# Optimization experiments

Hardware: AMD Instinct MI355X
Metric: run time of the kernel (lower is better)

The kernel has to match this reference:

```python
import jax, jax.numpy as jnp
import numpy as np

Q_LATTICE = 4      # nested lattice alphabet size
QMAX_ACT = 127.0   # 2**(8-1) - 1 for 8-bit LSQ


def _lattice_quantize(x_blocks, G, Ginv, q):
    # x_blocks: [N, 8] rows are block vectors. Lattice point = z @ G, z integer.
    z = jnp.round(x_blocks @ Ginv)
    half = q // 2
    z_mod = jnp.mod(z + half, q) - half  # nested (mod-q) lattice, centered
    return z_mod @ G


def setup_inputs() -> dict:
    key = jax.random.key(0)
    k1, k2 = jax.random.split(key)
    O, I, BS = 4096, 4096, 8
    rng = np.random.default_rng(0)
    G_np = np.eye(BS, dtype=np.float64) + 0.1 * rng.standard_normal((BS, BS))
    Ginv_np = np.linalg.inv(G_np)
    return {
        "x": jax.random.normal(k1, (256, I), dtype=jnp.float32),
        "weight": jax.random.normal(k2, (O, I), dtype=jnp.float32),
        "bias": jnp.zeros((O,), dtype=jnp.float32),
        "theta_beta": jnp.ones((O, 1), dtype=jnp.float32),
        "alpha": jnp.ones((1,), dtype=jnp.float32),
        "G": jnp.asarray(G_np, dtype=jnp.float32),
        "Ginv": jnp.asarray(Ginv_np, dtype=jnp.float32),
    }


def reference(x, weight, bias, theta_beta, alpha, G, Ginv):
    O, I = weight.shape
    bs = G.shape[0]
    nblk = I // bs
    sg = jax.lax.stop_gradient

    # --- hierarchical nested-lattice weight quantization (row tiling) ---
    W_blocks = weight.reshape(O, nblk, bs)
    # theta_beta [O, k] -> mean over k -> [O, 1, 1], broadcast to all blocks
    scale_w = jnp.mean(theta_beta, axis=-1, keepdims=True)[:, None, :]
    W_scaled = (W_blocks * scale_w).reshape(-1, bs)
    # straight-through lattice quantize
    W_q = W_scaled + sg(_lattice_quantize(W_scaled, G, Ginv, Q_LATTICE) - W_scaled)
    W_q = W_q.reshape(O, I)

    # --- linear ---
    y = x @ W_q.T + bias

    # --- LSQ activation quantization ---
    a = jax.nn.relu(alpha) + 1e-8          # [1]
    y_clipped = y + sg(jnp.clip(y, -a, a) - y)  # ste_clip (clamp detached)
    s = a / QMAX_ACT
    y_scaled = y_clipped / s
    y_round = y_scaled + sg(jnp.round(y_scaled) - y_scaled)  # ste_round
    return y_round * s
```

## Files before the change

kernel.cpp:

```cpp
#include <hip/hip_runtime.h>

typedef __attribute__((ext_vector_type(8))) __bf16 bf16x8;
typedef __attribute__((ext_vector_type(4))) float f32x4;

#define M_ 256
#define N_ 4096
#define K_ 4096
#define SPLITK 4
#define KC (K_ / SPLITK)
#define BM 256
#define BN 64
#define BK 32
#define KSTEPS (KC / BK)
#define NCH 36
#define LDSBUF 36864



__device__ __forceinline__ unsigned short f2bf(float f) {
  unsigned int u = __builtin_bit_cast(unsigned int, f);
  u += 0x7fffu + ((u >> 16) & 1u);
  return (unsigned short)(u >> 16);
}

__device__ __forceinline__ void async16(const void* g, void* l) {
  __builtin_amdgcn_global_load_lds(
      (const __attribute__((address_space(1))) unsigned int*)g,
      (__attribute__((address_space(3))) unsigned int*)l, 16, 0, 0);
}

__device__ __forceinline__ float lsq1(float y, float a, float s) {
  float yc = fminf(fmaxf(y, -a), a);
  return rintf(yc / s) * s;
}

#define ZLUT 0x3F800000BF80C000ull

__device__ __forceinline__ uint4 zdec(unsigned int w) {
  unsigned int d[4];
#pragma unroll
  for (int p = 0; p < 4; ++p) {
    const unsigned int lo = (unsigned int)((ZLUT >> (((w >> (4 * p)) & 3u) * 16)) & 0xFFFFull);
    const unsigned int hi = (unsigned int)((ZLUT >> (((w >> (4 * p + 2)) & 3u) * 16)) & 0xFFFFull);
    d[p] = lo | (hi << 16);
  }
  return make_uint4(d[0], d[1], d[2], d[3]);
}


#define NQB ((N_ * K_ / 8) / 256)
#define NXB ((M_ * K_ / 8) / 256)

__global__ __launch_bounds__(256) void k_prep(const float* __restrict__ W,
                                              const float* __restrict__ theta,
                                              const float* __restrict__ Ginv,
                                              const float* __restrict__ x,
                                              const float* __restrict__ G,
                                              unsigned short* __restrict__ z2,
                                              unsigned short* __restrict__ hi,
                                              unsigned short* __restrict__ lo,
                                              int kTheta) {
  __shared__ float Ms[64];
  const int tid = threadIdx.x;
  const bool isQ = blockIdx.x < NQB;
  if (tid < 64) Ms[tid] = isQ ? Ginv[tid] : G[tid];
  __syncthreads();

  if (isQ) {
#pragma clang fp contract(off)
    const int s = blockIdx.x * 256 + tid;
    const int lane6 = s & 63;
    const int tile = s >> 6;
    const int o  = ((tile >> 7) << 4) + (lane6 & 15);
    const int kb = ((tile & 127) << 2) + (lane6 >> 4);
    const float4* wp = (const float4*)(W + ((size_t)o << 12) + ((size_t)kb << 3));
    const float4 w0 = wp[0], w1 = wp[1];
    float sc = 0.f;
    for (int t = 0; t < kTheta; ++t) sc += theta[o * kTheta + t];
    sc /= (float)kTheta;
    const float wsv[8] = {w0.x * sc, w0.y * sc, w0.z * sc, w0.w * sc,
                          w1.x * sc, w1.y * sc, w1.z * sc, w1.w * sc};
    unsigned int word = 0u;
#pragma unroll
    for (int i = 0; i < 8; ++i) {
      float t = 0.f;
#pragma unroll
      for (int j = 0; j < 8; ++j)
        t = t + wsv[j] * Ms[j * 8 + i];
      const int zi = (int)rintf(t);
      word |= (unsigned int)((zi + 2) & 3) << (2 * i);
    }
    z2[s] = (unsigned short)word;
  } else {
    const int s = (blockIdx.x - NQB) * 256 + tid;
    const int lane6 = s & 63;
    const int tile = s >> 6;
    const int m  = ((tile >> 7) << 4) + (lane6 & 15);
    const int kb = ((tile & 127) << 2) + (lane6 >> 4);
    const float4* xp = (const float4*)(x + ((size_t)m << 12) + ((size_t)kb << 3));
    const float4 a0 = xp[0], a1 = xp[1];
    float xv[8] = {a0.x, a0.y, a0.z, a0.w, a1.x, a1.y, a1.z, a1.w};
    unsigned int ph[4] = {0u, 0u, 0u, 0u}, pl[4] = {0u, 0u, 0u, 0u};
#pragma unroll
    for (int i = 0; i < 8; ++i) {
      float t = 0.f;
#pragma unroll
      for (int j = 0; j < 8; ++j) t = fmaf(xv[j], Ms[i * 8 + j], t);
      const unsigned short hb = f2bf(t);
      const float hf = __builtin_bit_cast(float, (unsigned int)hb << 16);
      const unsigned short lb = f2bf(t - hf);
      ph[i >> 1] |= ((unsigned int)hb) << ((i & 1) * 16);
      pl[i >> 1] |= ((unsigned int)lb) << ((i & 1) * 16);
    }
    *(uint4*)(hi + ((size_t)s << 3)) = make_uint4(ph[0], ph[1], ph[2], ph[3]);
    *(uint4*)(lo + ((size_t)s << 3)) = make_uint4(pl[0], pl[1], pl[2], pl[3]);
  }
}


__global__ __launch_bounds__(512, 2) void k_gemm(const unsigned short* __restrict__ xgh,
                                                 const unsigned short* __restrict__ xgl,
                                                 const unsigned short* __restrict__ z2,
                                                 float* __restrict__ part) {
  __shared__ uint4 smem4[2 * LDSBUF / 16];
  char* smem = (char*)smem4;

  const int tid = threadIdx.x;
  const int lane = tid & 63, wave = tid >> 6;
  const int b = blockIdx.x;
  const int sk = b & 3;
  const int nt = b >> 2;
  const int k0t = sk * (KC / 32);
  const int lrow = lane & 15, lkg = lane >> 4;

  const unsigned short* asrc[4];
  int aldo[4];
#pragma unroll
  for (int ci = 0; ci < 4; ++ci) {
    const int c = wave * 4 + ci;
    const unsigned short* P = (c < 16) ? xgh : xgl;
    const int rt = c & 15;
    asrc[ci] = P + (((size_t)(rt * 128 + k0t)) << 9) + lane * 8;
    aldo[ci] = c * 1024;
  }
  const bool brole = (wave < 4);
  const unsigned short* zsrc = nullptr;
  int bofs = 0;
  if (brole) {
    zsrc = z2 + (((size_t)((nt * 4 + wave) * 128 + k0t)) << 6) + lane;
    bofs = (32 + wave) * 1024 + lane * 16;
  }

  f32x4 acc[2][4] = {};

  unsigned int zw = 0;
#pragma unroll
  for (int ci = 0; ci < 4; ++ci) async16(asrc[ci], smem + aldo[ci]);
  if (brole) {
    zw = zsrc[0];
    *(uint4*)(smem + bofs) = zdec(zw);
    zw = zsrc[64];
  }
  __syncthreads();

  for (int ks = 0; ks < KSTEPS; ++ks) {
    const int cur = (ks & 1) * LDSBUF;
    const int nxt = LDSBUF - cur;
    if (ks + 1 < KSTEPS) {
#pragma unroll
      for (int ci = 0; ci < 4; ++ci)
        async16(asrc[ci] + (size_t)(ks + 1) * 512, smem + nxt + aldo[ci]);
      if (brole) {
        *(uint4*)(smem + nxt + bofs) = zdec(zw);
        if (ks + 2 < KSTEPS) zw = zsrc[(size_t)(ks + 2) * 64];
      }
    }

    bf16x8 ah[2], al[2], bfr[4];
#pragma unroll
    for (int mf = 0; mf < 2; ++mf) {
      ah[mf] = *(const bf16x8*)(smem + cur + (wave * 2 + mf) * 1024 + lane * 16);
      al[mf] = *(const bf16x8*)(smem + cur + 16384 + (wave * 2 + mf) * 1024 + lane * 16);
    }
#pragma unroll
    for (int nf = 0; nf < 4; ++nf)
      bfr[nf] = *(const bf16x8*)(smem + cur + 32768 + nf * 1024 + lane * 16);

#pragma unroll
    for (int mf = 0; mf < 2; ++mf)
#pragma unroll
      for (int nf = 0; nf < 4; ++nf) {
        acc[mf][nf] = __builtin_amdgcn_mfma_f32_16x16x32_bf16(ah[mf], bfr[nf], acc[mf][nf], 0, 0, 0);
        acc[mf][nf] = __builtin_amdgcn_mfma_f32_16x16x32_bf16(al[mf], bfr[nf], acc[mf][nf], 0, 0, 0);
      }
    __syncthreads();
  }

  float* pb = part + (size_t)sk * (M_ * N_);
#pragma unroll
  for (int mf = 0; mf < 2; ++mf)
#pragma unroll
    for (int nf = 0; nf < 4; ++nf)
#pragma unroll
      for (int r = 0; r < 4; ++r) {
        const int m = wave * 32 + mf * 16 + lkg * 4 + r;
        const int n = nt * BN + nf * 16 + lrow;
        pb[(size_t)m * N_ + n] = acc[mf][nf][r];
      }
}


__global__ __launch_bounds__(256) void k_epi(const float* __restrict__ part,
                                             const float* __restrict__ bias,
                                             const float* __restrict__ alpha,
                                             float* __restrict__ out) {
  const int i4 = blockIdx.x * 256 + threadIdx.x;
  const size_t off = (size_t)i4 * 4;
  const float4 p0 = *(const float4*)(part + off);
  const float4 p1 = *(const float4*)(part + (size_t)1 * M_ * N_ + off);
  const float4 p2 = *(const float4*)(part + (size_t)2 * M_ * N_ + off);
  const float4 p3 = *(const float4*)(part + (size_t)3 * M_ * N_ + off);
  const int n = (int)(off & (N_ - 1));
  const float4 bv = *(const float4*)(bias + n);
  const float a = fmaxf(alpha[0], 0.f) + 1e-8f;
  const float s = a / 127.0f;
  float4 o;
  o.x = lsq1(((p0.x + p1.x) + p2.x) + p3.x + bv.x, a, s);
  o.y = lsq1(((p0.y + p1.y) + p2.y) + p3.y + bv.y, a, s);
  o.z = lsq1(((p0.z + p1.z) + p2.z) + p3.z + bv.z, a, s);
  o.w = lsq1(((p0.w + p1.w) + p2.w) + p3.w + bv.w, a, s);
  *(float4*)(out + off) = o;
}


extern "C" void kernel_launch(void* const* d_in, const int* in_sizes, int n_in,
                              void* d_out, int out_size, void* d_ws, size_t ws_size,
                              hipStream_t stream) {
  const float* x     = (const float*)d_in[0];
  const float* W     = (const float*)d_in[1];
  const float* bias  = (const float*)d_in[2];
  const float* theta = (const float*)d_in[3];
  const float* alpha = (const float*)d_in[4];
  const float* G     = (const float*)d_in[5];
  const float* Ginv  = (const float*)d_in[6];
  float* out = (float*)d_out;

  const int O = in_sizes[2];
  const int kTheta = in_sizes[3] / O;

  char* ws = (char*)d_ws;
  unsigned short* xgh = (unsigned short*)ws;
  unsigned short* xgl = (unsigned short*)(ws + 2097152);
  unsigned short* z2  = (unsigned short*)(ws + 4194304);
  float* part = (float*)(ws + 8388608);
  if (ws_size < 25165824) return;

  k_prep<<<NQB + NXB, 256, 0, stream>>>(W, theta, Ginv, x, G, z2, xgh, xgl, kTheta);
  k_gemm<<<SPLITK * (N_ / BN), 512, 0, stream>>>(xgh, xgl, z2, part);
  k_epi<<<(M_ * N_ / 4) / 256, 256, 0, stream>>>(part, bias, alpha, out);
}
```

Baseline: 52.46 us.

## Widen GEMM N-tile to 128 with 2x4 wave grid and split-K of 8

Doubles the block N-tile so each wave computes a 64x64 sub-tile in a 4x2 wave layout, and all eight waves now help decode the lattice-coded B operand. Split-K rises from 4 to 8 so the grid stays at 256 blocks. The goal is more MFMA work per A-tile load from LDS, so the hi/lo activation tiles are reused across twice as many columns. The cost is twice the partial-sum traffic (8 fp32 slices written and re-read by the epilogue), a larger workspace, more accumulator registers per thread, and half as many K-steps per block.

```diff
diff --git a/kernel.cpp b/kernel.cpp
--- a/kernel.cpp
+++ b/kernel.cpp
@@ -6,14 +6,13 @@
 #define M_ 256
 #define N_ 4096
 #define K_ 4096
-#define SPLITK 4
+#define SPLITK 8
 #define KC (K_ / SPLITK)
 #define BM 256
-#define BN 64
+#define BN 128
 #define BK 32
 #define KSTEPS (KC / BK)
-#define NCH 36
-#define LDSBUF 36864
+#define LDSBUF 40960
 
 
 
@@ -127,9 +126,10 @@
 
   const int tid = threadIdx.x;
   const int lane = tid & 63, wave = tid >> 6;
+  const int wr = wave >> 1, wc = wave & 1;
   const int b = blockIdx.x;
-  const int sk = b & 3;
-  const int nt = b >> 2;
+  const int sk = b & 7;
+  const int nt = b >> 3;
   const int k0t = sk * (KC / 32);
   const int lrow = lane & 15, lkg = lane >> 4;
 
@@ -143,24 +143,16 @@
     asrc[ci] = P + (((size_t)(rt * 128 + k0t)) << 9) + lane * 8;
     aldo[ci] = c * 1024;
   }
-  const bool brole = (wave < 4);
-  const unsigned short* zsrc = nullptr;
-  int bofs = 0;
-  if (brole) {
-    zsrc = z2 + (((size_t)((nt * 4 + wave) * 128 + k0t)) << 6) + lane;
-    bofs = (32 + wave) * 1024 + lane * 16;
-  }
-
-  f32x4 acc[2][4] = {};
-
-  unsigned int zw = 0;
+  const unsigned short* zsrc = z2 + (((size_t)((nt * 8 + wave) * 128 + k0t)) << 6) + lane;
+  const int bofs = (32 + wave) * 1024 + lane * 16;
+
+  f32x4 acc[4][4] = {};
+
 #pragma unroll
   for (int ci = 0; ci < 4; ++ci) async16(asrc[ci], smem + aldo[ci]);
-  if (brole) {
-    zw = zsrc[0];
-    *(uint4*)(smem + bofs) = zdec(zw);
-    zw = zsrc[64];
-  }
+  unsigned int zw = zsrc[0];
+  *(uint4*)(smem + bofs) = zdec(zw);
+  zw = zsrc[64];
   __syncthreads();
 
   for (int ks = 0; ks < KSTEPS; ++ks) {
@@ -170,24 +162,22 @@
 #pragma unroll
       for (int ci = 0; ci < 4; ++ci)
         async16(asrc[ci] + (size_t)(ks + 1) * 512, smem + nxt + aldo[ci]);
-      if (brole) {
-        *(uint4*)(smem + nxt + bofs) = zdec(zw);
-        if (ks + 2 < KSTEPS) zw = zsrc[(size_t)(ks + 2) * 64];
-      }
-    }
-
-    bf16x8 ah[2], al[2], bfr[4];
-#pragma unroll
-    for (int mf = 0; mf < 2; ++mf) {
-      ah[mf] = *(const bf16x8*)(smem + cur + (wave * 2 + mf) * 1024 + lane * 16);
-      al[mf] = *(const bf16x8*)(smem + cur + 16384 + (wave * 2 + mf) * 1024 + lane * 16);
+      *(uint4*)(smem + nxt + bofs) = zdec(zw);
+      if (ks + 2 < KSTEPS) zw = zsrc[(size_t)(ks + 2) * 64];
+    }
+
+    bf16x8 ah[4], al[4], bfr[4];
+#pragma unroll
+    for (int mf = 0; mf < 4; ++mf) {
+      ah[mf] = *(const bf16x8*)(smem + cur + (wr * 4 + mf) * 1024 + lane * 16);
+      al[mf] = *(const bf16x8*)(smem + cur + 16384 + (wr * 4 + mf) * 1024 + lane * 16);
     }
 #pragma unroll
     for (int nf = 0; nf < 4; ++nf)
-      bfr[nf] = *(const bf16x8*)(smem + cur + 32768 + nf * 1024 + lane * 16);
-
-#pragma unroll
-    for (int mf = 0; mf < 2; ++mf)
+      bfr[nf] = *(const bf16x8*)(smem + cur + 32768 + (wc * 4 + nf) * 1024 + lane * 16);
+
+#pragma unroll
+    for (int mf = 0; mf < 4; ++mf)
 #pragma unroll
       for (int nf = 0; nf < 4; ++nf) {
         acc[mf][nf] = __builtin_amdgcn_mfma_f32_16x16x32_bf16(ah[mf], bfr[nf], acc[mf][nf], 0, 0, 0);
@@ -198,13 +188,13 @@
 
   float* pb = part + (size_t)sk * (M_ * N_);
 #pragma unroll
-  for (int mf = 0; mf < 2; ++mf)
+  for (int mf = 0; mf < 4; ++mf)
 #pragma unroll
     for (int nf = 0; nf < 4; ++nf)
 #pragma unroll
       for (int r = 0; r < 4; ++r) {
-        const int m = wave * 32 + mf * 16 + lkg * 4 + r;
-        const int n = nt * BN + nf * 16 + lrow;
+        const int m = wr * 64 + mf * 16 + lkg * 4 + r;
+        const int n = nt * BN + wc * 64 + nf * 16 + lrow;
         pb[(size_t)m * N_ + n] = acc[mf][nf][r];
       }
 }
@@ -216,19 +206,21 @@
                                              float* __restrict__ out) {
   const int i4 = blockIdx.x * 256 + threadIdx.x;
   const size_t off = (size_t)i4 * 4;
-  const float4 p0 = *(const float4*)(part + off);
-  const float4 p1 = *(const float4*)(part + (size_t)1 * M_ * N_ + off);
-  const float4 p2 = *(const float4*)(part + (size_t)2 * M_ * N_ + off);
-  const float4 p3 = *(const float4*)(part + (size_t)3 * M_ * N_ + off);
+  float4 acc = *(const float4*)(part + off);
+#pragma unroll
+  for (int p = 1; p < SPLITK; ++p) {
+    const float4 q = *(const float4*)(part + (size_t)p * M_ * N_ + off);
+    acc.x += q.x; acc.y += q.y; acc.z += q.z; acc.w += q.w;
+  }
   const int n = (int)(off & (N_ - 1));
   const float4 bv = *(const float4*)(bias + n);
   const float a = fmaxf(alpha[0], 0.f) + 1e-8f;
   const float s = a / 127.0f;
   float4 o;
-  o.x = lsq1(((p0.x + p1.x) + p2.x) + p3.x + bv.x, a, s);
-  o.y = lsq1(((p0.y + p1.y) + p2.y) + p3.y + bv.y, a, s);
-  o.z = lsq1(((p0.z + p1.z) + p2.z) + p3.z + bv.z, a, s);
-  o.w = lsq1(((p0.w + p1.w) + p2.w) + p3.w + bv.w, a, s);
+  o.x = lsq1(acc.x + bv.x, a, s);
+  o.y = lsq1(acc.y + bv.y, a, s);
+  o.z = lsq1(acc.z + bv.z, a, s);
+  o.w = lsq1(acc.w + bv.w, a, s);
   *(float4*)(out + off) = o;
 }
 
@@ -253,7 +245,7 @@
   unsigned short* xgl = (unsigned short*)(ws + 2097152);
   unsigned short* z2  = (unsigned short*)(ws + 4194304);
   float* part = (float*)(ws + 8388608);
-  if (ws_size < 25165824) return;
+  if (ws_size < 41943040) return;
 
   k_prep<<<NQB + NXB, 256, 0, stream>>>(W, theta, Ginv, x, G, z2, xgh, xgl, kTheta);
   k_gemm<<<SPLITK * (N_ / BN), 512, 0, stream>>>(xgh, xgl, z2, part);
```

Measured after the change: 51.42 us. -2.0%, faster.
